# Optimization experiments

Measured on AMD Instinct MI355X. Metric: run time of the kernel, lower is better.

## Reference

```python
import jax, jax.numpy as jnp
import numpy as np

D_MODEL = 1024
D_STATE = 128
SEQ_LEN = 4096
BATCH = 4
N_FFT = 2 ** int(np.ceil(np.log2(2 * SEQ_LEN - 1)))  # 8192
LN_EPS = 1e-3  # keras LayerNormalization default epsilon


def setup_inputs() -> dict:
    key = jax.random.key(0)
    ks = jax.random.split(key, 12)
    def dense_w(k, fan_in, fan_out):
        lim = np.sqrt(6.0 / (fan_in + fan_out)).astype(np.float32)  # glorot uniform
        return jax.random.uniform(k, (fan_in, fan_out), jnp.float32, -lim, lim)
    return {
        "x": jax.random.normal(ks[0], (BATCH, SEQ_LEN, D_MODEL), jnp.float32),
        "ln_gamma": jnp.ones((D_MODEL,), jnp.float32),
        "ln_beta": jnp.zeros((D_MODEL,), jnp.float32),
        "W_in": dense_w(ks[1], D_MODEL, D_MODEL),
        "b_in": jnp.zeros((D_MODEL,), jnp.float32),
        "W_xs": dense_w(ks[2], D_MODEL, D_STATE),
        "W_B": dense_w(ks[3], D_MODEL, D_STATE),
        "b_B": jnp.zeros((D_STATE,), jnp.float32),
        "W_C": dense_w(ks[4], D_MODEL, D_STATE),
        "b_C": jnp.zeros((D_STATE,), jnp.float32),
        "A_log": jax.random.uniform(ks[5], (D_STATE,), jnp.float32, -4.0, -1.0),
        "D": jnp.ones((D_MODEL,), jnp.float32),
        "W_so": dense_w(ks[6], D_STATE, D_MODEL),
        "W_out": dense_w(ks[7], D_MODEL, D_MODEL),
        "b_out": jnp.zeros((D_MODEL,), jnp.float32),
    }


def reference(x, ln_gamma, ln_beta, W_in, b_in, W_xs, W_B, b_B, W_C, b_C,
              A_log, D, W_so, W_out, b_out):
    residual = x
    # LayerNorm over last dim
    mu = jnp.mean(x, axis=-1, keepdims=True)
    var = jnp.mean(jnp.square(x - mu), axis=-1, keepdims=True)
    xn = (x - mu) * jax.lax.rsqrt(var + LN_EPS) * ln_gamma + ln_beta
    # projections
    z = xn @ W_in + b_in                      # [B, L, d_model]
    x_state = z @ W_xs                        # [B, L, d_state]
    B_sel = z @ W_B + b_B                     # [B, L, d_state]
    C_sel = z @ W_C + b_C                     # [B, L, d_state]
    # stable A-parameterization -> kernel K[t, s] = exp(A_s * t)
    A = -jnp.exp(A_log)                       # [d_state]
    t = jnp.arange(SEQ_LEN, dtype=jnp.float32)
    K = jnp.exp(t[:, None] * A[None, :])      # [L, d_state]
    # FFT convolution along time axis (zero-padded to N_FFT, causal slice)
    u = x_state * B_sel                       # [B, L, d_state]
    u_f = jnp.fft.rfft(u, n=N_FFT, axis=1)    # [B, N_FFT//2+1, d_state]
    k_f = jnp.fft.rfft(K, n=N_FFT, axis=0)    # [N_FFT//2+1, d_state]
    y_state = jnp.fft.irfft(u_f * k_f[None], n=N_FFT, axis=1)[:, :SEQ_LEN]
    y_state = y_state * C_sel
    # output path with skip connection through D
    y = y_state @ W_so + D * z                # [B, L, d_model]
    y = y @ W_out + b_out
    return y + residual
```

## Files before the change

kernel.cpp:

```cpp
#include <hip/hip_runtime.h>
#include <math.h>

#define D_MODEL 1024
#define D_STATE 128
#define SEQ_LEN 4096
#define BATCH 4
#define NTOK (BATCH * SEQ_LEN)
#define LN_EPS 1e-3f
#define NCHUNK 128
#define LCHUNK (SEQ_LEN / NCHUNK)

typedef __attribute__((ext_vector_type(8))) short bf16x8;
typedef __attribute__((ext_vector_type(4))) float f32x4;

__device__ __forceinline__ short f2bf(float f) {
    union { float f; unsigned u; } v; v.f = f;
    unsigned r = v.u + 0x7FFFu + ((v.u >> 16) & 1u);
    return (short)(r >> 16);
}
__device__ __forceinline__ float bf2f(short s) {
    union { unsigned u; float f; } v; v.u = ((unsigned)(unsigned short)s) << 16;
    return v.f;
}

__global__ __launch_bounds__(256) void ln_kernel(const float* __restrict__ x,
                                                 const float* __restrict__ gamma,
                                                 const float* __restrict__ beta,
                                                 short* __restrict__ xn_bf) {
    int row = blockIdx.x;
    const float4* xr = (const float4*)(x + (size_t)row * D_MODEL);
    float4 v = xr[threadIdx.x];
    float s1 = v.x + v.y + v.z + v.w;
    float s2 = v.x * v.x + v.y * v.y + v.z * v.z + v.w * v.w;
    for (int off = 32; off; off >>= 1) {
        s1 += __shfl_down(s1, off);
        s2 += __shfl_down(s2, off);
    }
    __shared__ float ls1[4], ls2[4];
    int wid = threadIdx.x >> 6, lane = threadIdx.x & 63;
    if (lane == 0) { ls1[wid] = s1; ls2[wid] = s2; }
    __syncthreads();
    s1 = ls1[0] + ls1[1] + ls1[2] + ls1[3];
    s2 = ls2[0] + ls2[1] + ls2[2] + ls2[3];
    float mu = s1 * (1.0f / D_MODEL);
    float var = s2 * (1.0f / D_MODEL) - mu * mu;
    float r = rsqrtf(var + LN_EPS);
    float4 g = ((const float4*)gamma)[threadIdx.x];
    float4 b = ((const float4*)beta)[threadIdx.x];
    short4 o;
    o.x = f2bf((v.x - mu) * r * g.x + b.x);
    o.y = f2bf((v.y - mu) * r * g.y + b.y);
    o.z = f2bf((v.z - mu) * r * g.z + b.z);
    o.w = f2bf((v.w - mu) * r * g.w + b.w);
    ((short4*)(xn_bf + (size_t)row * D_MODEL))[threadIdx.x] = o;
}

__global__ __launch_bounds__(256) void prep_kernel(
    const float* __restrict__ W_in, const float* __restrict__ W_xs,
    const float* __restrict__ W_B, const float* __restrict__ W_C,
    const float* __restrict__ W_so, const float* __restrict__ W_out,
    const float* __restrict__ bB, const float* __restrict__ bC,
    short* __restrict__ W_inT, short* __restrict__ W3T,
    short* __restrict__ W_soT, short* __restrict__ W_outT,
    float* __restrict__ bias3) {
    int blk = blockIdx.x;
    const float* in; short* out; int K, N, tile;
    if (blk < 1024)      { in = W_in;  out = W_inT;           K = 1024; N = 1024; tile = blk; }
    else if (blk < 1152) { in = W_xs;  out = W3T;             K = 1024; N = 128;  tile = blk - 1024; }
    else if (blk < 1280) { in = W_B;   out = W3T + 128*1024;  K = 1024; N = 128;  tile = blk - 1152; }
    else if (blk < 1408) { in = W_C;   out = W3T + 256*1024;  K = 1024; N = 128;  tile = blk - 1280; }
    else if (blk < 1536) { in = W_so;  out = W_soT;           K = 128;  N = 1024; tile = blk - 1408; }
    else if (blk < 2560) { in = W_out; out = W_outT;          K = 1024; N = 1024; tile = blk - 1536; }
    else {
        int t = threadIdx.y * 32 + threadIdx.x;
        for (int n = t; n < 384; n += 256)
            bias3[n] = (n < 128) ? 0.f : ((n < 256) ? bB[n - 128] : bC[n - 256]);
        return;
    }
    __shared__ float t32[32][33];
    int ntiles = N / 32;
    int nb = (tile % ntiles) * 32, kb = (tile / ntiles) * 32;
    int tx = threadIdx.x, ty = threadIdx.y;
#pragma unroll
    for (int i = 0; i < 4; ++i)
        t32[ty + 8 * i][tx] = in[(size_t)(kb + ty + 8 * i) * N + nb + tx];
    __syncthreads();
#pragma unroll
    for (int i = 0; i < 4; ++i)
        out[(size_t)(nb + ty + 8 * i) * K + kb + tx] = f2bf(t32[tx][ty + 8 * i]);
}

template<int HAS_BIAS, int HAS_ADD, int ADD_BF, int HAS_SCALE, int OUT_F32, int OUT_BF, int SWZ>
__global__ __launch_bounds__(256, 4) void gemm_bf16(
    const short* __restrict__ A, const short* __restrict__ BT,
    const float* __restrict__ bias,
    const float* __restrict__ addf, const short* __restrict__ addb,
    const float* __restrict__ addscale,
    float* __restrict__ Cf, short* __restrict__ Cbf,
    int Mt, int Nt, int K) {
    __shared__ short As[128 * 64];
    __shared__ short Bs[128 * 64];
    int p = blockIdx.x;
    int mtile, ntile;
    if (SWZ) {
        int k = p & 7, q = p >> 3;
        ntile = q & 7;
        mtile = k + 8 * (q >> 3);
    } else {
        mtile = p % Mt;
        ntile = p / Mt;
    }
    int m0 = mtile * 128, n0 = ntile * 128;
    int N = Nt * 128;
    int tid = threadIdx.x;
    int lane = tid & 63;
    int w = tid >> 6;
    int quad = lane >> 4, r16 = lane & 15;
    int wm = (w & 1) * 64, wn = (w >> 1) * 64;

    f32x4 acc[4][4] = {};

    for (int k0 = 0; k0 < K; k0 += 64) {
#pragma unroll
        for (int it = 0; it < 4; ++it) {
            int seg = it * 256 + tid;
            int row = seg >> 3, slot = seg & 7;
            int kc8 = slot ^ (row & 7);
            const short* gp = A + (size_t)(m0 + row) * K + k0 + kc8 * 8;
            __builtin_amdgcn_global_load_lds(
                (const __attribute__((address_space(1))) unsigned*)gp,
                (__attribute__((address_space(3))) unsigned*)(As + seg * 8), 16, 0, 0);
        }
#pragma unroll
        for (int it = 0; it < 4; ++it) {
            int seg = it * 256 + tid;
            int row = seg >> 3, slot = seg & 7;
            int kc8 = slot ^ (row & 7);
            const short* gp = BT + (size_t)(n0 + row) * K + k0 + kc8 * 8;
            __builtin_amdgcn_global_load_lds(
                (const __attribute__((address_space(1))) unsigned*)gp,
                (__attribute__((address_space(3))) unsigned*)(Bs + seg * 8), 16, 0, 0);
        }
        __syncthreads();

        const short* abase = As + (wm + r16) * 64;
        const short* bbase = Bs + (wn + r16) * 64;
        int sw = r16 & 7;
#pragma unroll
        for (int kk = 0; kk < 2; ++kk) {
            int phys = ((quad + 4 * kk) ^ sw) * 8;
            bf16x8 af[4], bfr[4];
#pragma unroll
            for (int i = 0; i < 4; ++i) af[i] = *(const bf16x8*)(abase + i * 16 * 64 + phys);
#pragma unroll
            for (int j = 0; j < 4; ++j) bfr[j] = *(const bf16x8*)(bbase + j * 16 * 64 + phys);
#pragma unroll
            for (int i = 0; i < 4; ++i)
#pragma unroll
                for (int j = 0; j < 4; ++j)
                    acc[i][j] = __builtin_amdgcn_mfma_f32_16x16x32_bf16(af[i], bfr[j], acc[i][j], 0, 0, 0);
        }
        __syncthreads();
    }

#pragma unroll
    for (int i = 0; i < 4; ++i) {
#pragma unroll
        for (int j = 0; j < 4; ++j) {
            int col = n0 + wn + j * 16 + r16;
            float bv = HAS_BIAS ? bias[col] : 0.f;
            float sc = HAS_SCALE ? addscale[col] : 1.f;
#pragma unroll
            for (int pr = 0; pr < 4; ++pr) {
                int row = m0 + wm + i * 16 + quad * 4 + pr;
                float v = acc[i][j][pr] + bv;
                if (HAS_ADD) {
                    float av = ADD_BF ? bf2f(addb[(size_t)row * N + col])
                                      : addf[(size_t)row * N + col];
                    v += sc * av;
                }
                if (OUT_F32) Cf[(size_t)row * N + col] = v;
                if (OUT_BF) Cbf[(size_t)row * N + col] = f2bf(v);
            }
        }
    }
}

__global__ __launch_bounds__(128) void scan_p1(const float* __restrict__ s3,
                                               const float* __restrict__ A_log,
                                               float* __restrict__ hbuf,
                                               float* __restrict__ Ebuf) {
    int s = threadIdx.x;
    int c = blockIdx.x, b = blockIdx.y;
    float a = expf(-expf(A_log[s]));
    float h = 0.f;
    size_t base = (size_t)b * SEQ_LEN + (size_t)c * LCHUNK;
#pragma unroll 8
    for (int i = 0; i < LCHUNK; ++i) {
        size_t r = base + i;
        float u = s3[r * 384 + s] * s3[r * 384 + 128 + s];
        h = a * h + u;
        hbuf[r * 128 + s] = h;
    }
    Ebuf[((size_t)b * NCHUNK + c) * 128 + s] = h;
}

__global__ __launch_bounds__(512) void scan_p2(const float* __restrict__ A_log,
                                               const float* __restrict__ Ebuf,
                                               float* __restrict__ Gbuf) {
    int tid = threadIdx.x;
    int b = tid >> 7, s = tid & 127;
    float pw = expf(-expf(A_log[s]) * (float)LCHUNK);
    float G = 0.f;
    for (int c0 = 0; c0 < NCHUNK; c0 += 16) {
        float e[16];
#pragma unroll
        for (int t = 0; t < 16; ++t)
            e[t] = Ebuf[((size_t)b * NCHUNK + c0 + t) * 128 + s];
#pragma unroll
        for (int t = 0; t < 16; ++t) {
            G = pw * G + e[t];
            Gbuf[((size_t)b * NCHUNK + c0 + t) * 128 + s] = G;
        }
    }
}

__global__ __launch_bounds__(128) void scan_p3(const float* __restrict__ s3,
                                               const float* __restrict__ A_log,
                                               const float* __restrict__ hbuf,
                                               const float* __restrict__ Gbuf,
                                               short* __restrict__ ys_bf) {
    int s = threadIdx.x;
    int c = blockIdx.x, b = blockIdx.y;
    float a = expf(-expf(A_log[s]));
    float carry = (c == 0) ? 0.f : Gbuf[((size_t)b * NCHUNK + c - 1) * 128 + s];
    float p = a;
    size_t base = (size_t)b * SEQ_LEN + (size_t)c * LCHUNK;
#pragma unroll 8
    for (int i = 0; i < LCHUNK; ++i) {
        size_t r = base + i;
        float h = hbuf[r * 128 + s] + p * carry;
        p *= a;
        ys_bf[r * 128 + s] = f2bf(h * s3[r * 384 + 256 + s]);
    }
}

extern "C" void kernel_launch(void* const* d_in, const int* in_sizes, int n_in,
                              void* d_out, int out_size, void* d_ws, size_t ws_size,
                              hipStream_t stream) {
    const float* x     = (const float*)d_in[0];
    const float* ln_g  = (const float*)d_in[1];
    const float* ln_b  = (const float*)d_in[2];
    const float* W_in  = (const float*)d_in[3];
    const float* b_in  = (const float*)d_in[4];
    const float* W_xs  = (const float*)d_in[5];
    const float* W_B   = (const float*)d_in[6];
    const float* b_B   = (const float*)d_in[7];
    const float* W_C   = (const float*)d_in[8];
    const float* b_C   = (const float*)d_in[9];
    const float* A_log = (const float*)d_in[10];
    const float* Dvec  = (const float*)d_in[11];
    const float* W_so  = (const float*)d_in[12];
    const float* W_out = (const float*)d_in[13];
    const float* b_out = (const float*)d_in[14];
    float* out = (float*)d_out;

    char* w = (char*)d_ws;
    size_t off = 0;
    short* xn_bf = (short*)(w + off);
    float* hbuf  = (float*)(w + off);
    short* ys_bf = (short*)(w + off + 8388608);
    off += (size_t)NTOK * D_MODEL * 2;
    short* z_bf  = (short*)(w + off);
    off += (size_t)NTOK * D_MODEL * 2;
    short* y1_bf = (short*)(w + off);
    off += (size_t)NTOK * D_MODEL * 2;
    float* s3    = (float*)(w + off); off += (size_t)NTOK * 384 * 4;
    float* Ebuf  = (float*)(w + off); off += (size_t)BATCH * NCHUNK * 128 * 4;
    float* Gbuf  = (float*)(w + off); off += (size_t)BATCH * NCHUNK * 128 * 4;
    short* W_inT  = (short*)(w + off); off += (size_t)D_MODEL * D_MODEL * 2;
    short* W3T    = (short*)(w + off); off += (size_t)384 * D_MODEL * 2;
    short* W_soT  = (short*)(w + off); off += (size_t)D_MODEL * D_STATE * 2;
    short* W_outT = (short*)(w + off); off += (size_t)D_MODEL * D_MODEL * 2;
    float* bias3  = (float*)(w + off); off += 2048;

    prep_kernel<<<2561, dim3(32, 8), 0, stream>>>(W_in, W_xs, W_B, W_C, W_so, W_out,
                                                  b_B, b_C, W_inT, W3T, W_soT, W_outT, bias3);

    ln_kernel<<<NTOK, 256, 0, stream>>>(x, ln_g, ln_b, xn_bf);

    const int Mt = NTOK / 128;
    gemm_bf16<1, 0, 0, 0, 0, 1, 1><<<Mt * 8, 256, 0, stream>>>(
        xn_bf, W_inT, b_in, nullptr, nullptr, nullptr,
        nullptr, z_bf, Mt, 8, D_MODEL);

    gemm_bf16<1, 0, 0, 0, 1, 0, 0><<<Mt * 3, 256, 0, stream>>>(
        z_bf, W3T, bias3, nullptr, nullptr, nullptr,
        s3, nullptr, Mt, 3, D_MODEL);

    scan_p1<<<dim3(NCHUNK, BATCH), 128, 0, stream>>>(s3, A_log, hbuf, Ebuf);
    scan_p2<<<1, 512, 0, stream>>>(A_log, Ebuf, Gbuf);
    scan_p3<<<dim3(NCHUNK, BATCH), 128, 0, stream>>>(s3, A_log, hbuf, Gbuf, ys_bf);

    gemm_bf16<0, 1, 1, 1, 0, 1, 1><<<Mt * 8, 256, 0, stream>>>(
        ys_bf, W_soT, nullptr, nullptr, z_bf, Dvec,
        nullptr, y1_bf, Mt, 8, D_STATE);

    gemm_bf16<1, 1, 0, 0, 1, 0, 1><<<Mt * 8, 256, 0, stream>>>(
        y1_bf, W_outT, b_out, x, nullptr, nullptr,
        out, nullptr, Mt, 8, D_MODEL);
}
```

Before: 282.3 us.

## Stage GEMM epilogue through LDS for coalesced vector stores; merge LN into prep

The GEMM epilogue now writes each 16-row slice of the accumulator into shared memory and reads it back row-wise, so global loads of the residual/add inputs and the output stores become coalesced float4/short4 accesses instead of scattered scalar ones. The layer-norm kernel is folded into the weight-prep kernel as extra blocks, saving one launch. The tile swizzle is generalised to arbitrary Nt, and the 3-wide projection GEMM now uses the XCD-aware swizzle. The epilogue adds extra barriers and LDS round-trips per slice.

```diff
diff --git a/kernel.cpp b/kernel.cpp
--- a/kernel.cpp
+++ b/kernel.cpp
@@ -23,47 +23,47 @@
     return v.f;
 }
 
-__global__ __launch_bounds__(256) void ln_kernel(const float* __restrict__ x,
-                                                 const float* __restrict__ gamma,
-                                                 const float* __restrict__ beta,
-                                                 short* __restrict__ xn_bf) {
-    int row = blockIdx.x;
-    const float4* xr = (const float4*)(x + (size_t)row * D_MODEL);
-    float4 v = xr[threadIdx.x];
-    float s1 = v.x + v.y + v.z + v.w;
-    float s2 = v.x * v.x + v.y * v.y + v.z * v.z + v.w * v.w;
-    for (int off = 32; off; off >>= 1) {
-        s1 += __shfl_down(s1, off);
-        s2 += __shfl_down(s2, off);
-    }
-    __shared__ float ls1[4], ls2[4];
-    int wid = threadIdx.x >> 6, lane = threadIdx.x & 63;
-    if (lane == 0) { ls1[wid] = s1; ls2[wid] = s2; }
-    __syncthreads();
-    s1 = ls1[0] + ls1[1] + ls1[2] + ls1[3];
-    s2 = ls2[0] + ls2[1] + ls2[2] + ls2[3];
-    float mu = s1 * (1.0f / D_MODEL);
-    float var = s2 * (1.0f / D_MODEL) - mu * mu;
-    float r = rsqrtf(var + LN_EPS);
-    float4 g = ((const float4*)gamma)[threadIdx.x];
-    float4 b = ((const float4*)beta)[threadIdx.x];
-    short4 o;
-    o.x = f2bf((v.x - mu) * r * g.x + b.x);
-    o.y = f2bf((v.y - mu) * r * g.y + b.y);
-    o.z = f2bf((v.z - mu) * r * g.z + b.z);
-    o.w = f2bf((v.w - mu) * r * g.w + b.w);
-    ((short4*)(xn_bf + (size_t)row * D_MODEL))[threadIdx.x] = o;
-}
-
-__global__ __launch_bounds__(256) void prep_kernel(
+__global__ __launch_bounds__(256) void prep_ln_kernel(
     const float* __restrict__ W_in, const float* __restrict__ W_xs,
     const float* __restrict__ W_B, const float* __restrict__ W_C,
     const float* __restrict__ W_so, const float* __restrict__ W_out,
     const float* __restrict__ bB, const float* __restrict__ bC,
     short* __restrict__ W_inT, short* __restrict__ W3T,
     short* __restrict__ W_soT, short* __restrict__ W_outT,
-    float* __restrict__ bias3) {
+    float* __restrict__ bias3,
+    const float* __restrict__ x, const float* __restrict__ gamma,
+    const float* __restrict__ beta, short* __restrict__ xn_bf) {
     int blk = blockIdx.x;
+    if (blk >= 2561) {
+        int row = blk - 2561;
+        int t = threadIdx.y * 32 + threadIdx.x;
+        const float4* xr = (const float4*)(x + (size_t)row * D_MODEL);
+        float4 v = xr[t];
+        float s1 = v.x + v.y + v.z + v.w;
+        float s2 = v.x * v.x + v.y * v.y + v.z * v.z + v.w * v.w;
+        for (int off = 32; off; off >>= 1) {
+            s1 += __shfl_down(s1, off);
+            s2 += __shfl_down(s2, off);
+        }
+        __shared__ float ls1[4], ls2[4];
+        int wid = t >> 6, lane = t & 63;
+        if (lane == 0) { ls1[wid] = s1; ls2[wid] = s2; }
+        __syncthreads();
+        s1 = ls1[0] + ls1[1] + ls1[2] + ls1[3];
+        s2 = ls2[0] + ls2[1] + ls2[2] + ls2[3];
+        float mu = s1 * (1.0f / D_MODEL);
+        float var = s2 * (1.0f / D_MODEL) - mu * mu;
+        float r = rsqrtf(var + LN_EPS);
+        float4 g = ((const float4*)gamma)[t];
+        float4 b = ((const float4*)beta)[t];
+        short4 o;
+        o.x = f2bf((v.x - mu) * r * g.x + b.x);
+        o.y = f2bf((v.y - mu) * r * g.y + b.y);
+        o.z = f2bf((v.z - mu) * r * g.z + b.z);
+        o.w = f2bf((v.w - mu) * r * g.w + b.w);
+        ((short4*)(xn_bf + (size_t)row * D_MODEL))[t] = o;
+        return;
+    }
     const float* in; short* out; int K, N, tile;
     if (blk < 1024)      { in = W_in;  out = W_inT;           K = 1024; N = 1024; tile = blk; }
     else if (blk < 1152) { in = W_xs;  out = W3T;             K = 1024; N = 128;  tile = blk - 1024; }
@@ -98,14 +98,15 @@
     const float* __restrict__ addscale,
     float* __restrict__ Cf, short* __restrict__ Cbf,
     int Mt, int Nt, int K) {
-    __shared__ short As[128 * 64];
-    __shared__ short Bs[128 * 64];
+    __shared__ short LDSH[2 * 128 * 64];
+    short* As = LDSH;
+    short* Bs = LDSH + 128 * 64;
     int p = blockIdx.x;
     int mtile, ntile;
     if (SWZ) {
-        int k = p & 7, q = p >> 3;
-        ntile = q & 7;
-        mtile = k + 8 * (q >> 3);
+        int xcd = p & 7, q = p >> 3;
+        ntile = q % Nt;
+        mtile = xcd + 8 * (q / Nt);
     } else {
         mtile = p % Mt;
         ntile = p / Mt;
@@ -163,24 +164,47 @@
         __syncthreads();
     }
 
-#pragma unroll
-    for (int i = 0; i < 4; ++i) {
-#pragma unroll
-        for (int j = 0; j < 4; ++j) {
-            int col = n0 + wn + j * 16 + r16;
-            float bv = HAS_BIAS ? bias[col] : 0.f;
-            float sc = HAS_SCALE ? addscale[col] : 1.f;
-#pragma unroll
-            for (int pr = 0; pr < 4; ++pr) {
-                int row = m0 + wm + i * 16 + quad * 4 + pr;
-                float v = acc[i][j][pr] + bv;
-                if (HAS_ADD) {
-                    float av = ADD_BF ? bf2f(addb[(size_t)row * N + col])
-                                      : addf[(size_t)row * N + col];
-                    v += sc * av;
+    float* ep = (float*)LDSH;
+    int cw = (tid & 31) * 4;
+    int lrw = (w & 1) * 16;
+    int pcb = (w >> 1) * 64;
+    float4 b4 = {0.f, 0.f, 0.f, 0.f};
+    float4 sc4 = {1.f, 1.f, 1.f, 1.f};
+    if (HAS_BIAS) b4 = *(const float4*)(bias + n0 + cw);
+    if (HAS_SCALE) sc4 = *(const float4*)(addscale + n0 + cw);
+#pragma unroll
+    for (int ih = 0; ih < 4; ++ih) {
+        __syncthreads();
+#pragma unroll
+        for (int j = 0; j < 4; ++j)
+#pragma unroll
+            for (int pr = 0; pr < 4; ++pr)
+                ep[(lrw + quad * 4 + pr) * 136 + pcb + j * 16 + r16] = acc[ih][j][pr];
+        __syncthreads();
+#pragma unroll
+        for (int rb = 0; rb < 4; ++rb) {
+            int lr = rb * 8 + (tid >> 5);
+            int grow = m0 + ((lr >> 4) << 6) + ih * 16 + (lr & 15);
+            size_t goff = (size_t)grow * N + n0 + cw;
+            float4 v = *(const float4*)(ep + lr * 136 + cw);
+            if (HAS_BIAS) { v.x += b4.x; v.y += b4.y; v.z += b4.z; v.w += b4.w; }
+            if (HAS_ADD) {
+                float ax, ay, az, aw;
+                if (ADD_BF) {
+                    short4 ab = *(const short4*)(addb + goff);
+                    ax = bf2f(ab.x); ay = bf2f(ab.y); az = bf2f(ab.z); aw = bf2f(ab.w);
+                } else {
+                    float4 af4 = *(const float4*)(addf + goff);
+                    ax = af4.x; ay = af4.y; az = af4.z; aw = af4.w;
                 }
-                if (OUT_F32) Cf[(size_t)row * N + col] = v;
-                if (OUT_BF) Cbf[(size_t)row * N + col] = f2bf(v);
+                v.x += sc4.x * ax; v.y += sc4.y * ay;
+                v.z += sc4.z * az; v.w += sc4.w * aw;
+            }
+            if (OUT_F32) *(float4*)(Cf + goff) = v;
+            if (OUT_BF) {
+                short4 o;
+                o.x = f2bf(v.x); o.y = f2bf(v.y); o.z = f2bf(v.z); o.w = f2bf(v.w);
+                *(short4*)(Cbf + goff) = o;
             }
         }
     }
@@ -284,17 +308,17 @@
     short* W_outT = (short*)(w + off); off += (size_t)D_MODEL * D_MODEL * 2;
     float* bias3  = (float*)(w + off); off += 2048;
 
-    prep_kernel<<<2561, dim3(32, 8), 0, stream>>>(W_in, W_xs, W_B, W_C, W_so, W_out,
-                                                  b_B, b_C, W_inT, W3T, W_soT, W_outT, bias3);
-
-    ln_kernel<<<NTOK, 256, 0, stream>>>(x, ln_g, ln_b, xn_bf);
+    prep_ln_kernel<<<2561 + NTOK, dim3(32, 8), 0, stream>>>(
+        W_in, W_xs, W_B, W_C, W_so, W_out, b_B, b_C,
+        W_inT, W3T, W_soT, W_outT, bias3,
+        x, ln_g, ln_b, xn_bf);
 
     const int Mt = NTOK / 128;
     gemm_bf16<1, 0, 0, 0, 0, 1, 1><<<Mt * 8, 256, 0, stream>>>(
         xn_bf, W_inT, b_in, nullptr, nullptr, nullptr,
         nullptr, z_bf, Mt, 8, D_MODEL);
 
-    gemm_bf16<1, 0, 0, 0, 1, 0, 0><<<Mt * 3, 256, 0, stream>>>(
+    gemm_bf16<1, 0, 0, 0, 1, 0, 1><<<Mt * 3, 256, 0, stream>>>(
         z_bf, W3T, bias3, nullptr, nullptr, nullptr,
         s3, nullptr, Mt, 3, D_MODEL);
 
```

New measurement: 276.9 us. About the same (-1.9%).
